# Kernel optimization log

Measured on AMD Instinct MI355X. Metric: run time of the kernel, lower is better.

## Reference

```python
import jax, jax.numpy as jnp
import numpy as np

DOT_TEMP = 0.05  # hardcoded in the original forward (self.temperature is never used)
EPS = 1e-6


def setup_inputs() -> dict:
    key = jax.random.key(0)
    k1, k2 = jax.random.split(key)
    bsz, n_views, dim = 4096, 2, 128
    features = jax.random.normal(k1, (bsz, n_views, dim), dtype=jnp.float32)
    labels = jax.random.randint(k2, (bsz,), 0, 100, dtype=jnp.int32)
    return {"features": features, "labels": labels}


def reference(features, labels):
    bsz, V, dim = features.shape  # V = n_views; contrast_mode='all' -> anchor_count = contrast_count = V
    n = V * bsz

    # contrast_feature = cat(unbind(features, dim=1), dim=0): [view0 batch; view1 batch; ...]
    cf = jnp.transpose(features, (1, 0, 2)).reshape(n, dim)  # [n, dim]

    # positive mask: eq(labels, labels.T) tiled, diagonal zeroed
    eq = labels[:, None] == labels[None, :]  # [bsz, bsz]
    mask = jnp.tile(eq.astype(jnp.float32), (V, V))  # [n, n]
    mask = mask * (1.0 - jnp.eye(n, dtype=jnp.float32))

    # Key simplification (exactly faithful): mask3[i] (eq) and mask2[i] (ne) are complementary,
    # so unique(cat(where(mask3[i]), where(mask2[i]))) == arange(n) for every row. Hence each
    # loop iteration in the original computes the SAME scalar from the full gram matrix.
    lab2 = jnp.tile(labels, V)  # matches labels2[:n] layout in the original
    diff = (lab2[:, None] != lab2[None, :]).astype(jnp.float32)  # [n, n]

    dots = jnp.matmul(cf, cf.T) / DOT_TEMP  # [n, n]
    dm = dots * diff
    maxd = jnp.max(dm, axis=1, keepdims=True)
    S = jnp.sum(jnp.exp(dm - maxd))  # exp_terms.sum() -- identical for every valid row
    N = jnp.sum(diff)                # different_label_mask.sum()

    # rows with mask2[i].sum() == 0 are skipped (left at zero)
    valid = jnp.tile(jnp.any(labels[None, :] != labels[:, None], axis=1), V)  # [n]
    xv = jnp.where(valid, S, 0.0)
    nv = jnp.where(valid, N, 0.0)

    # if not all(negtivesum == 0): x = x / negtivesum   (safe divide for skipped rows)
    all_zero = jnp.all(nv == 0.0)
    xv = jnp.where(all_zero, xv, xv / jnp.where(nv == 0.0, 1.0, nv))

    log_prob = -jnp.log(xv[:, None] + EPS)  # [n, 1], broadcast over columns
    msum = jnp.sum(mask, axis=1)
    msum_safe = jnp.where(msum == 0.0, 1.0, msum)
    pos_logits = -jnp.sum(mask * log_prob, axis=1) / msum_safe  # [n]
    loss = jnp.mean(pos_logits)  # mean over view(anchor_count, bsz) == overall mean
    return loss
```

## Files before the change

### kernel.cpp

```cpp
#include <hip/hip_runtime.h>
#include <hip/hip_bf16.h>
#include <stdint.h>

#define N_TOT 8192
#define BSZ   4096
#define NCH   32
#define SQS   5.3715827f

typedef _Float16 f16x8 __attribute__((ext_vector_type(8)));
typedef float f32x4 __attribute__((ext_vector_type(4)));

__device__ __forceinline__ float fast_exp2(float x) {
#if __has_builtin(__builtin_amdgcn_exp2f)
  return __builtin_amdgcn_exp2f(x);
#else
  return exp2f(x);
#endif
}
#define EXP2(x) fast_exp2(x)

__global__ __launch_bounds__(256) void prep16_kernel(
    const float* __restrict__ feat, const int* __restrict__ labels,
    _Float16* __restrict__ H2, unsigned char* __restrict__ lab8, int* __restrict__ cnt,
    int* __restrict__ ctr) {
  if (blockIdx.x == 512) {
    __shared__ int h[128];
    if (threadIdx.x < 128) h[threadIdx.x] = 0;
    __syncthreads();
    for (int i = threadIdx.x; i < BSZ; i += 256) atomicAdd(&h[labels[i] & 127], 1);
    __syncthreads();
    if (threadIdx.x < 128) cnt[threadIdx.x] = h[threadIdx.x];
    if (threadIdx.x == 0) *ctr = 0;
    for (int i = threadIdx.x; i < N_TOT; i += 256)
      lab8[i] = (unsigned char)labels[i & (BSZ - 1)];
    return;
  }
  int idx = blockIdx.x * 256 + threadIdx.x;
  int rowblk = idx >> 8, inner = idx & 255;
  int k8 = inner >> 4, rlo = inner & 15;
  int r = rowblk * 16 + rlo;
  int b = r & (BSZ - 1), v = r >> 12;
  const float* src = feat + ((size_t)((b << 1) + v) << 7) + k8 * 8;
  float4 x0 = *(const float4*)src;
  float4 x1 = *(const float4*)(src + 4);
  float xs[8] = {x0.x, x0.y, x0.z, x0.w, x1.x, x1.y, x1.z, x1.w};
  f16x8 hv;
#pragma unroll
  for (int jj = 0; jj < 8; ++jj) hv[jj] = (_Float16)(xs[jj] * SQS);
  *(f16x8*)((char*)H2 + (size_t)idx * 16) = hv;
}

__global__ __launch_bounds__(256, 4) void gemm16_kernel(
    const _Float16* __restrict__ H2, const unsigned char* __restrict__ lab8,
    float* __restrict__ pM, float* __restrict__ pS) {
  __shared__ __align__(16) char ldsB[2][16384];

  int orig = blockIdx.x;
  int xcd = orig & 7, j = orig >> 3;
  int cg = xcd * 4 + (j & 3);
  int rg = j >> 2;
  int wave = threadIdx.x >> 6, lane = threadIdx.x & 63;
  int lq = lane >> 4, lr16 = lane & 15;

  const uint32_t rowbase = (uint32_t)rg * 128 + wave * 32;
  const char* Hb = (const char*)H2;
  const uint32_t laneoff = lq * 256 + lr16 * 16;

  int lrw[2];
#pragma unroll
  for (int m = 0; m < 2; ++m)
    lrw[m] = lab8[rowbase + m * 16 + lr16];

  f16x8 Areg[2][4];
#pragma unroll
  for (int m = 0; m < 2; ++m)
#pragma unroll
    for (int kb = 0; kb < 4; ++kb)
      Areg[m][kb] = *(const f16x8*)(Hb + (size_t)((rowbase >> 4) + m) * 4096 + kb * 1024 + laneoff);

  const char* Bsrc = Hb + (size_t)cg * 65536;

#define STAGE(T, BUF)                                                                     \
  {                                                                                       \
    _Pragma("unroll")                                                                     \
    for (int i = 0; i < 4; ++i) {                                                         \
      int chunk = wave * 4 + i;                                                           \
      __builtin_amdgcn_global_load_lds(                                                   \
          (const __attribute__((address_space(1))) void*)(Bsrc + ((T) * 4 + (chunk >> 2)) * 4096 + (chunk & 3) * 1024 + lane * 16), \
          (__attribute__((address_space(3))) void*)(&ldsB[BUF][chunk * 1024]), 16, 0, 0); \
    }                                                                                     \
  }

  STAGE(0, 0);
  asm volatile("s_waitcnt vmcnt(0)" ::: "memory");
  __builtin_amdgcn_sched_barrier(0);
  __builtin_amdgcn_s_barrier();

  f32x4 acc[2][4];
  float mxv[2] = {-3.0e38f, -3.0e38f}, sv[2] = {0.0f, 0.0f};

#pragma unroll
  for (int t = 0; t < 4; ++t) {
    if (t < 3) STAGE(t + 1, (t + 1) & 1);
    const char* Bb = ldsB[t & 1];

#pragma unroll
    for (int m = 0; m < 2; ++m)
#pragma unroll
      for (int ni = 0; ni < 4; ++ni) acc[m][ni] = f32x4{0.f, 0.f, 0.f, 0.f};

#pragma unroll
    for (int kb = 0; kb < 4; ++kb) {
      f16x8 Bf[4];
#pragma unroll
      for (int ni = 0; ni < 4; ++ni)
        Bf[ni] = *(const f16x8*)(Bb + ni * 4096 + kb * 1024 + laneoff);
      __builtin_amdgcn_s_setprio(1);
#pragma unroll
      for (int m = 0; m < 2; ++m)
#pragma unroll
        for (int ni = 0; ni < 4; ++ni)
          acc[m][ni] = __builtin_amdgcn_mfma_f32_16x16x32_f16(Bf[ni], Areg[m][kb], acc[m][ni], 0, 0, 0);
      __builtin_amdgcn_s_setprio(0);
    }

    uint32_t labw[4];
#pragma unroll
    for (int ni = 0; ni < 4; ++ni)
      labw[ni] = *(const uint32_t*)(lab8 + cg * 256 + t * 64 + ni * 16 + lq * 4);

#pragma unroll
    for (int ni = 0; ni < 4; ++ni)
#pragma unroll
      for (int r = 0; r < 4; ++r) {
        int lc = (labw[ni] >> (8 * r)) & 255;
        acc[0][ni][r] = (lrw[0] != lc) ? acc[0][ni][r] : 0.0f;
        acc[1][ni][r] = (lrw[1] != lc) ? acc[1][ni][r] : 0.0f;
      }

#pragma unroll
    for (int m = 0; m < 2; ++m) {
      float b0 = fmaxf(fmaxf(acc[m][0][0], acc[m][0][1]), fmaxf(acc[m][0][2], acc[m][0][3]));
      float b1 = fmaxf(fmaxf(acc[m][1][0], acc[m][1][1]), fmaxf(acc[m][1][2], acc[m][1][3]));
      float b2 = fmaxf(fmaxf(acc[m][2][0], acc[m][2][1]), fmaxf(acc[m][2][2], acc[m][2][3]));
      float b3 = fmaxf(fmaxf(acc[m][3][0], acc[m][3][1]), fmaxf(acc[m][3][2], acc[m][3][3]));
      float bm = fmaxf(fmaxf(b0, b1), fmaxf(b2, b3));
      float nm = fmaxf(mxv[m], bm);
      float s0 = 0.f, s1 = 0.f, s2 = 0.f, s3 = 0.f;
#pragma unroll
      for (int r = 0; r < 4; ++r) {
        s0 += EXP2(acc[m][0][r] - nm);
        s1 += EXP2(acc[m][1][r] - nm);
        s2 += EXP2(acc[m][2][r] - nm);
        s3 += EXP2(acc[m][3][r] - nm);
      }
      sv[m] = sv[m] * EXP2(mxv[m] - nm) + ((s0 + s1) + (s2 + s3));
      mxv[m] = nm;
    }

    asm volatile("s_waitcnt vmcnt(0)" ::: "memory");
    __builtin_amdgcn_sched_barrier(0);
    __builtin_amdgcn_s_barrier();
  }
#undef STAGE

#pragma unroll
  for (int m = 0; m < 2; ++m) {
    float M = mxv[m], S = sv[m];
#pragma unroll
    for (int off = 16; off < 64; off <<= 1) {
      float Mo = __shfl_xor(M, off, 64);
      float So = __shfl_xor(S, off, 64);
      float Mn = fmaxf(M, Mo);
      S = S * EXP2(M - Mn) + So * EXP2(Mo - Mn);
      M = Mn;
    }
    if (lane < 16) {
      pM[(size_t)cg * N_TOT + rowbase + m * 16 + lane] = M;
      pS[(size_t)cg * N_TOT + rowbase + m * 16 + lane] = S;
    }
  }
}

__global__ __launch_bounds__(256) void rowredfinal16_kernel(
    const float* __restrict__ pM, const float* __restrict__ pS,
    const int* __restrict__ cnt, float* __restrict__ blockS,
    int* __restrict__ ctr, float* __restrict__ out) {
  int row = blockIdx.x * 256 + threadIdx.x;
  float M = -3.0e38f;
#pragma unroll
  for (int c = 0; c < NCH; ++c) M = fmaxf(M, pM[(size_t)c * N_TOT + row]);
  float s = 0.0f;
#pragma unroll
  for (int c = 0; c < NCH; ++c)
    s += pS[(size_t)c * N_TOT + row] * EXP2(pM[(size_t)c * N_TOT + row] - M);
  __shared__ float red[256];
  red[threadIdx.x] = s;
  __syncthreads();
  for (int st = 128; st > 0; st >>= 1) {
    if (threadIdx.x < st) red[threadIdx.x] += red[threadIdx.x + st];
    __syncthreads();
  }
  if (threadIdx.x == 0) {
    blockS[blockIdx.x] = red[0];
    __threadfence();
    int old = atomicAdd(ctr, 1);
    if (old == 31) {
      __threadfence();
      double Stot = 0.0;
      for (int b2 = 0; b2 < 32; ++b2) Stot += (double)blockS[b2];
      long long sumsq = 0;
      int nval = 0;
      for (int c = 0; c < 128; ++c) {
        long long cc = cnt[c];
        sumsq += cc * cc;
        if (cc > 0 && cc < BSZ) nval += 2 * (int)cc;
      }
      double Nd = (double)N_TOT * (double)N_TOT - 4.0 * (double)sumsq;
      float loss;
      if (Nd <= 0.0 || nval == 0) {
        loss = logf(1e-6f);
      } else {
        float x = (float)(Stot / Nd);
        loss = ((float)nval * logf(x + 1e-6f) +
                (float)(N_TOT - nval) * logf(1e-6f)) / (float)N_TOT;
      }
      out[0] = loss;
    }
  }
}

extern "C" void kernel_launch(void* const* d_in, const int* in_sizes, int n_in,
                              void* d_out, int out_size, void* d_ws, size_t ws_size,
                              hipStream_t stream) {
  const float* feat = (const float*)d_in[0];
  const int* labels = (const int*)d_in[1];
  float* out = (float*)d_out;

  char* ws = (char*)d_ws;
  _Float16* H2        = (_Float16*)(ws);
  unsigned char* lab8 = (unsigned char*)(ws + 2097152);
  float* pM           = (float*)(ws + 2105344);
  float* pS           = (float*)(ws + 3153920);
  int* cnt            = (int*)(ws + 4202496);
  float* blockS       = (float*)(ws + 4203008);
  int* ctr            = (int*)(ws + 4203136);

  prep16_kernel<<<513, 256, 0, stream>>>(feat, labels, H2, lab8, cnt, ctr);
  gemm16_kernel<<<2048, 256, 0, stream>>>(H2, lab8, pM, pS);
  rowredfinal16_kernel<<<32, 256, 0, stream>>>(pM, pS, cnt, blockS, ctr, out);
}
```

Measured before the change: 54.58 us.

## Double each wave's row tile, halve the grid, and software-pipeline LDS fragment loads

Each wave now keeps 64 anchor rows (four 16-row fragments) in registers instead of 32, so the block covers 256 rows and the grid shrinks from 2048 to 1024 blocks. Each B tile staged in LDS is therefore reused across twice as many MFMAs. The code also restructures synchronisation: it waits with vmcnt(4) so the next stage's async global-to-LDS copies stay in flight, and it double-buffers the B fragments read from LDS across k-steps. The cost is more accumulator and A registers with the occupancy hint removed from launch_bounds, which may lower occupancy, and fewer blocks to spread over the CUs.

```diff
diff --git a/kernel.cpp b/kernel.cpp
--- a/kernel.cpp
+++ b/kernel.cpp
@@ -19,7 +19,7 @@
 }
 #define EXP2(x) fast_exp2(x)
 
-__global__ __launch_bounds__(256) void prep16_kernel(
+__global__ __launch_bounds__(256) void prep20_kernel(
     const float* __restrict__ feat, const int* __restrict__ labels,
     _Float16* __restrict__ H2, unsigned char* __restrict__ lab8, int* __restrict__ cnt,
     int* __restrict__ ctr) {
@@ -50,7 +50,7 @@
   *(f16x8*)((char*)H2 + (size_t)idx * 16) = hv;
 }
 
-__global__ __launch_bounds__(256, 4) void gemm16_kernel(
+__global__ __launch_bounds__(256) void gemm20_kernel(
     const _Float16* __restrict__ H2, const unsigned char* __restrict__ lab8,
     float* __restrict__ pM, float* __restrict__ pS) {
   __shared__ __align__(16) char ldsB[2][16384];
@@ -62,18 +62,18 @@
   int wave = threadIdx.x >> 6, lane = threadIdx.x & 63;
   int lq = lane >> 4, lr16 = lane & 15;
 
-  const uint32_t rowbase = (uint32_t)rg * 128 + wave * 32;
+  const uint32_t rowbase = (uint32_t)rg * 256 + wave * 64;
   const char* Hb = (const char*)H2;
   const uint32_t laneoff = lq * 256 + lr16 * 16;
 
-  int lrw[2];
-#pragma unroll
-  for (int m = 0; m < 2; ++m)
+  int lrw[4];
+#pragma unroll
+  for (int m = 0; m < 4; ++m)
     lrw[m] = lab8[rowbase + m * 16 + lr16];
 
-  f16x8 Areg[2][4];
-#pragma unroll
-  for (int m = 0; m < 2; ++m)
+  f16x8 Areg[4][4];
+#pragma unroll
+  for (int m = 0; m < 4; ++m)
 #pragma unroll
     for (int kb = 0; kb < 4; ++kb)
       Areg[m][kb] = *(const f16x8*)(Hb + (size_t)((rowbase >> 4) + m) * 4096 + kb * 1024 + laneoff);
@@ -92,35 +92,46 @@
   }
 
   STAGE(0, 0);
-  asm volatile("s_waitcnt vmcnt(0)" ::: "memory");
-  __builtin_amdgcn_sched_barrier(0);
-  __builtin_amdgcn_s_barrier();
-
-  f32x4 acc[2][4];
-  float mxv[2] = {-3.0e38f, -3.0e38f}, sv[2] = {0.0f, 0.0f};
+
+  f32x4 acc[4][4];
+  float mxv[4] = {-3.0e38f, -3.0e38f, -3.0e38f, -3.0e38f};
+  float sv[4] = {0.0f, 0.0f, 0.0f, 0.0f};
 
 #pragma unroll
   for (int t = 0; t < 4; ++t) {
-    if (t < 3) STAGE(t + 1, (t + 1) & 1);
+    if (t < 3) {
+      STAGE(t + 1, (t + 1) & 1);
+      asm volatile("s_waitcnt vmcnt(4)" ::: "memory");
+    } else {
+      asm volatile("s_waitcnt vmcnt(0)" ::: "memory");
+    }
+    __builtin_amdgcn_sched_barrier(0);
+    __builtin_amdgcn_s_barrier();
     const char* Bb = ldsB[t & 1];
 
 #pragma unroll
-    for (int m = 0; m < 2; ++m)
+    for (int m = 0; m < 4; ++m)
 #pragma unroll
       for (int ni = 0; ni < 4; ++ni) acc[m][ni] = f32x4{0.f, 0.f, 0.f, 0.f};
 
+    f16x8 Bf[2][4];
+#pragma unroll
+    for (int ni = 0; ni < 4; ++ni)
+      Bf[0][ni] = *(const f16x8*)(Bb + ni * 4096 + laneoff);
 #pragma unroll
     for (int kb = 0; kb < 4; ++kb) {
-      f16x8 Bf[4];
-#pragma unroll
-      for (int ni = 0; ni < 4; ++ni)
-        Bf[ni] = *(const f16x8*)(Bb + ni * 4096 + kb * 1024 + laneoff);
+      int cur = kb & 1;
+      if (kb < 3) {
+#pragma unroll
+        for (int ni = 0; ni < 4; ++ni)
+          Bf[cur ^ 1][ni] = *(const f16x8*)(Bb + ni * 4096 + (kb + 1) * 1024 + laneoff);
+      }
       __builtin_amdgcn_s_setprio(1);
 #pragma unroll
-      for (int m = 0; m < 2; ++m)
+      for (int m = 0; m < 4; ++m)
 #pragma unroll
         for (int ni = 0; ni < 4; ++ni)
-          acc[m][ni] = __builtin_amdgcn_mfma_f32_16x16x32_f16(Bf[ni], Areg[m][kb], acc[m][ni], 0, 0, 0);
+          acc[m][ni] = __builtin_amdgcn_mfma_f32_16x16x32_f16(Bf[cur][ni], Areg[m][kb], acc[m][ni], 0, 0, 0);
       __builtin_amdgcn_s_setprio(0);
     }
 
@@ -134,12 +145,13 @@
 #pragma unroll
       for (int r = 0; r < 4; ++r) {
         int lc = (labw[ni] >> (8 * r)) & 255;
-        acc[0][ni][r] = (lrw[0] != lc) ? acc[0][ni][r] : 0.0f;
-        acc[1][ni][r] = (lrw[1] != lc) ? acc[1][ni][r] : 0.0f;
-      }
-
-#pragma unroll
-    for (int m = 0; m < 2; ++m) {
+#pragma unroll
+        for (int m = 0; m < 4; ++m)
+          acc[m][ni][r] = (lrw[m] != lc) ? acc[m][ni][r] : 0.0f;
+      }
+
+#pragma unroll
+    for (int m = 0; m < 4; ++m) {
       float b0 = fmaxf(fmaxf(acc[m][0][0], acc[m][0][1]), fmaxf(acc[m][0][2], acc[m][0][3]));
       float b1 = fmaxf(fmaxf(acc[m][1][0], acc[m][1][1]), fmaxf(acc[m][1][2], acc[m][1][3]));
       float b2 = fmaxf(fmaxf(acc[m][2][0], acc[m][2][1]), fmaxf(acc[m][2][2], acc[m][2][3]));
@@ -158,14 +170,12 @@
       mxv[m] = nm;
     }
 
-    asm volatile("s_waitcnt vmcnt(0)" ::: "memory");
-    __builtin_amdgcn_sched_barrier(0);
     __builtin_amdgcn_s_barrier();
   }
 #undef STAGE
 
 #pragma unroll
-  for (int m = 0; m < 2; ++m) {
+  for (int m = 0; m < 4; ++m) {
     float M = mxv[m], S = sv[m];
 #pragma unroll
     for (int off = 16; off < 64; off <<= 1) {
@@ -182,7 +192,7 @@
   }
 }
 
-__global__ __launch_bounds__(256) void rowredfinal16_kernel(
+__global__ __launch_bounds__(256) void rowredfinal20_kernel(
     const float* __restrict__ pM, const float* __restrict__ pS,
     const int* __restrict__ cnt, float* __restrict__ blockS,
     int* __restrict__ ctr, float* __restrict__ out) {
@@ -246,7 +256,7 @@
   float* blockS       = (float*)(ws + 4203008);
   int* ctr            = (int*)(ws + 4203136);
 
-  prep16_kernel<<<513, 256, 0, stream>>>(feat, labels, H2, lab8, cnt, ctr);
-  gemm16_kernel<<<2048, 256, 0, stream>>>(H2, lab8, pM, pS);
-  rowredfinal16_kernel<<<32, 256, 0, stream>>>(pM, pS, cnt, blockS, ctr, out);
-}
+  prep20_kernel<<<513, 256, 0, stream>>>(feat, labels, H2, lab8, cnt, ctr);
+  gemm20_kernel<<<1024, 256, 0, stream>>>(H2, lab8, pM, pS);
+  rowredfinal20_kernel<<<32, 256, 0, stream>>>(pM, pS, cnt, blockS, ctr, out);
+}
```

Result: slower. 58.43 us (+7.1%).
